# Optimization experiments

Hardware: AMD Instinct MI355X
Metric: run time of the kernel (lower is better)

## Reference

```python
import jax, jax.numpy as jnp
import numpy as np

N = 100000      # nodes
E = 1600000     # edges
D_IN = 64       # input feature dim
H = 64          # hidden dim
HNUM = 128      # number of direct virtual nodes (blocks)
NCONV = 2       # layers-1 conv layers in module_list
NMLP = 2        # layers-1 virtual-node MLPs (all applied each conv iter)
NEG_SLOPE = 0.2


def setup_inputs() -> dict:
    key = jax.random.key(0)
    ks = jax.random.split(key, 16)
    s = 0.1
    inp = {
        "x": jax.random.normal(ks[0], (N, D_IN), jnp.float32),
        "edge_index": jax.random.randint(ks[1], (2, E), 0, N, dtype=jnp.int32),
        "h_blocks": jax.random.randint(ks[2], (N,), 0, HNUM, dtype=jnp.int32),
        "h_levels": jax.random.randint(ks[3], (N,), 0, 4, dtype=jnp.int32),
        "h_num": HNUM,
        # initial GATConv(input->hidden): lin weight (no bias), att_src, att_dst, out bias
        "W0": jax.random.normal(ks[4], (D_IN, H), jnp.float32) * s,
        "a_src0": jax.random.normal(ks[5], (H,), jnp.float32) * s,
        "a_dst0": jax.random.normal(ks[6], (H,), jnp.float32) * s,
        "b0": jnp.zeros((H,), jnp.float32),
        # stacked module_list GATConv(hidden->hidden) params
        "Wl": jax.random.normal(ks[7], (NCONV, H, H), jnp.float32) * s,
        "a_srcl": jax.random.normal(ks[8], (NCONV, H), jnp.float32) * s,
        "a_dstl": jax.random.normal(ks[9], (NCONV, H), jnp.float32) * s,
        "bl": jnp.zeros((NCONV, H), jnp.float32),
        # virtual node embedding, torch init constant 0
        "vn_emb": jnp.zeros((1, H), jnp.float32),
        # virtual-node MLPs: Linear->ReLU->Linear->ReLU, weights stored (in,out)
        "mlp_W1": jax.random.normal(ks[10], (NMLP, H, H), jnp.float32) * s,
        "mlp_b1": jnp.zeros((NMLP, H), jnp.float32),
        "mlp_W2": jax.random.normal(ks[11], (NMLP, H, H), jnp.float32) * s,
        "mlp_b2": jnp.zeros((NMLP, H), jnp.float32),
    }
    return inp


def gat_conv(x, src, dst, W, a_src, a_dst, b, n_nodes):
    """PyG GATConv, heads=1, concat, add_self_loops=True, negative_slope=0.2."""
    h = x @ W                                    # [N, H]
    loop = jnp.arange(n_nodes, dtype=src.dtype)
    s = jnp.concatenate([src, loop])             # [E+N]
    d = jnp.concatenate([dst, loop])
    a_s = h @ a_src                              # [N]
    a_d = h @ a_dst
    e = jax.nn.leaky_relu(a_s[s] + a_d[d], negative_slope=NEG_SLOPE)  # [E+N]
    # segment softmax over destination nodes (self loops cover every segment)
    m = jax.ops.segment_max(e, d, num_segments=n_nodes)
    w = jnp.exp(e - m[d])
    denom = jax.ops.segment_sum(w, d, num_segments=n_nodes)
    alpha = w / (denom[d] + 1e-16)               # [E+N]
    out = jax.ops.segment_sum(h[s] * alpha[:, None], d, num_segments=n_nodes)
    return out + b


def reference(x, edge_index, h_blocks, h_levels, h_num,
              W0, a_src0, a_dst0, b0, Wl, a_srcl, a_dstl, bl,
              vn_emb, mlp_W1, mlp_b1, mlp_W2, mlp_b2):
    src, dst = edge_index[0], edge_index[1]
    n_nodes = x.shape[0]
    out = gat_conv(x, src, dst, W0, a_src0, a_dst0, b0, n_nodes)
    # embedding lookup of all-zero indices == broadcast of row 0
    vn_direct = jnp.broadcast_to(vn_emb[0], (h_num, vn_emb.shape[1]))  # [HNUM, H]
    vn_root = vn_emb                                                   # [1, H]
    for l in range(NCONV):
        out = out + vn_direct[h_blocks]
        out = gat_conv(out, src, dst, Wl[l], a_srcl[l], a_dstl[l], bl[l], n_nodes)
        vn_direct = jax.ops.segment_sum(out, h_blocks, num_segments=h_num) + vn_direct
        vn_direct = vn_direct + vn_root
        vn_root = jnp.sum(vn_direct, axis=0, keepdims=True) + vn_root
        # NB: the original applies EVERY vn-MLP inside each conv iteration
        for j in range(NMLP):
            vn_direct = jax.nn.relu(jax.nn.relu(vn_direct @ mlp_W1[j] + mlp_b1[j]) @ mlp_W2[j] + mlp_b2[j])
            vn_root = jax.nn.relu(jax.nn.relu(vn_root @ mlp_W1[j] + mlp_b1[j]) @ mlp_W2[j] + mlp_b2[j])
    return out
```

## Files before the change

kernel.cpp:

```cpp
#include <hip/hip_runtime.h>
#include <hip/hip_fp16.h>
#include <math.h>

#define HD 64
#define HNUM 128
#define NMLP 2
#define BSH 8
#define MAXNB 512
#define EPB 2048
#define NPART 256

typedef unsigned int uint_t;
typedef unsigned short ushort_t;
typedef _Float16 h8 __attribute__((ext_vector_type(8)));
typedef float vf4 __attribute__((ext_vector_type(4)));

union H8U { h8 v; uint_t u[4]; };

__device__ __forceinline__ float lrelu(float x){ return fmaxf(x, 0.2f*x); }

__device__ __forceinline__ float cvt_h(uint_t wv, uint_t sh){
    __half_raw hr; hr.x = (ushort_t)(wv >> sh);
    return __half2float((__half)hr);
}
__device__ __forceinline__ uint_t pk2(float a, float b){
    return (uint_t)__half_as_ushort(__float2half_rn(a)) |
           ((uint_t)__half_as_ushort(__float2half_rn(b)) << 16);
}

__global__ __launch_bounds__(256) void k_bcnt(const int* __restrict__ dst, int* __restrict__ gb,
                                              int E, int NB){
    __shared__ int h[MAXNB];
    int t = threadIdx.x;
    for(int i=t;i<NB;i+=256) h[i] = 0;
    __syncthreads();
    for(int e = blockIdx.x*256 + t; e < E; e += gridDim.x*256)
        atomicAdd(&h[dst[e]>>BSH], 1);
    __syncthreads();
    for(int i=t;i<NB;i+=256) if(h[i]) atomicAdd(&gb[i], h[i]);
}

__global__ __launch_bounds__(512) void k_bscan(const int* __restrict__ gb, int* __restrict__ bbase,
                                               int* __restrict__ gcur, int NB){
    __shared__ int s[512];
    int t = threadIdx.x;
    int v = (t < NB) ? gb[t] : 0;
    s[t] = v; __syncthreads();
    for(int o=1;o<512;o<<=1){
        int u = (t >= o) ? s[t-o] : 0;
        __syncthreads();
        s[t] += u;
        __syncthreads();
    }
    if(t < NB){ int ex = s[t] - v; bbase[t] = ex; gcur[t] = ex; }
}

__global__ __launch_bounds__(256) void k_bin(const int* __restrict__ src, const int* __restrict__ dst,
                                             int* __restrict__ gcur, int2* __restrict__ bdata,
                                             int E, int NB){
    __shared__ int cnt[MAXNB];
    __shared__ int base[MAXNB];
    int t = threadIdx.x;
    for(int i=t;i<NB;i+=256) cnt[i] = 0;
    __syncthreads();
    int s0 = blockIdx.x*EPB;
    int sv[8], dv[8], off[8];
    #pragma unroll
    for(int i=0;i<8;i++){
        int e = s0 + i*256 + t;
        if(e < E){
            sv[i] = src[e]; dv[i] = dst[e];
            off[i] = atomicAdd(&cnt[dv[i]>>BSH], 1);
        }
    }
    __syncthreads();
    for(int i=t;i<NB;i+=256) base[i] = cnt[i] ? atomicAdd(&gcur[i], cnt[i]) : 0;
    __syncthreads();
    #pragma unroll
    for(int i=0;i<8;i++){
        int e = s0 + i*256 + t;
        if(e < E) bdata[base[dv[i]>>BSH] + off[i]] = make_int2(sv[i], dv[i]);
    }
}

__global__ __launch_bounds__(256) void k_bfuse(const int2* __restrict__ bdata, const int* __restrict__ bbase,
                                               const int* __restrict__ gb, int* __restrict__ rp,
                                               int* __restrict__ col, int n, int NB, int E){
    __shared__ int h[256];
    __shared__ int sc[256];
    int b = blockIdx.x, t = threadIdx.x;
    int beg = bbase[b], cnt = gb[b];
    h[t] = 0; __syncthreads();
    for(int i=t;i<cnt;i+=256) atomicAdd(&h[bdata[beg+i].y & 255], 1);
    __syncthreads();
    int v = h[t];
    sc[t] = v; __syncthreads();
    for(int o=1;o<256;o<<=1){
        int u = (t >= o) ? sc[t-o] : 0;
        __syncthreads();
        sc[t] += u;
        __syncthreads();
    }
    int excl = sc[t] - v;
    int node = (b<<BSH) + t;
    if(node < n) rp[node] = beg + excl;
    if(b == NB-1 && t == 255) rp[n] = E;
    __syncthreads();
    sc[t] = excl;
    __syncthreads();
    for(int i=t;i<cnt;i+=256){
        int2 e = bdata[beg+i];
        int pos = atomicAdd(&sc[e.y & 255], 1);
        col[beg + pos] = e.x;
    }
}

__global__ __launch_bounds__(256) void k_wcvt(
    const float* __restrict__ W0, const float* __restrict__ as0, const float* __restrict__ ad0,
    const float* __restrict__ Wl, const float* __restrict__ asl, const float* __restrict__ adl,
    uint4* __restrict__ Wf3, float* __restrict__ waf3)
{
    __shared__ float wa[2][64];
    int L = blockIdx.x, t = threadIdx.x;
    const float* W  = (L==0) ? W0  : Wl  + (L-1)*HD*HD;
    const float* as = (L==0) ? as0 : asl + (L-1)*HD;
    const float* ad = (L==0) ? ad0 : adl + (L-1)*HD;
    if(t < 128){
        int sd = t>>6, k = t&63;
        const float* av = sd ? ad : as;
        float acc = 0.f;
        for(int c=0;c<HD;c++) acc = fmaf(W[k*HD+c], av[c], acc);
        wa[sd][k] = acc;
    }
    __syncthreads();
    for(int it = t; it < 512; it += 256){
        int lane = it&63, s = (it>>6)&1, tile = it>>7;
        int g = lane>>4, m = lane&15, c = tile*16 + m;
        ushort_t h[8];
        #pragma unroll
        for(int i=0;i<8;i++){
            int k = s*32 + g*4 + (i&3) + 16*(i>>2);
            h[i] = __half_as_ushort(__float2half_rn(W[k*HD + c]));
        }
        uint4 q;
        q.x = (uint_t)h[0] | ((uint_t)h[1]<<16);
        q.y = (uint_t)h[2] | ((uint_t)h[3]<<16);
        q.z = (uint_t)h[4] | ((uint_t)h[5]<<16);
        q.w = (uint_t)h[6] | ((uint_t)h[7]<<16);
        Wf3[(size_t)L*512 + (tile*2+s)*64 + lane] = q;
    }
    if(t < 128){
        int lane = t&63, sd = t>>6, g = lane>>4;
        #pragma unroll
        for(int j4=0;j4<4;j4++){
            float v[4];
            #pragma unroll
            for(int e=0;e<4;e++){
                int j = j4*4 + e;
                int k = (j>>3)*32 + g*4 + (j&3) + 16*((j>>2)&1);
                v[e] = wa[sd][k];
            }
            float* dstp = waf3 + ((size_t)L*8 + sd*4 + j4)*64*4 + lane*4;
            dstp[0]=v[0]; dstp[1]=v[1]; dstp[2]=v[2]; dstp[3]=v[3];
        }
    }
}

__global__ __launch_bounds__(256) void k_gemm(
    const float* __restrict__ IN, const float* __restrict__ addrow,
    const float* __restrict__ addtab, const int* __restrict__ hb,
    const uint4* __restrict__ Wf, const float* __restrict__ waf,
    uint_t* __restrict__ Hw, float* __restrict__ AS, float* __restrict__ AD,
    int n)
{
    __shared__ ushort_t sx[4][1024];
    int t = threadIdx.x, lane = t&63, wv = t>>6;
    int g = lane>>4, m = lane&15;
    ushort_t* sb = sx[wv];

    H8U B[8];
    #pragma unroll
    for(int f=0; f<8; f++){
        uint4 q = Wf[f*64 + lane];
        B[f].u[0]=q.x; B[f].u[1]=q.y; B[f].u[2]=q.z; B[f].u[3]=q.w;
    }
    vf4 wS[4], wD[4];
    #pragma unroll
    for(int j4=0;j4<4;j4++){
        const float* ps = waf + ((size_t)0*4 + j4)*256 + lane*4;
        const float* pd = waf + ((size_t)1*4 + j4)*256 + lane*4;
        wS[j4] = vf4{ps[0],ps[1],ps[2],ps[3]};
        wD[j4] = vf4{pd[0],pd[1],pd[2],pd[3]};
    }
    float ar0=0,ar1=0,ar2=0,ar3=0;
    if(addrow){
        const float* a = &addrow[m*4];
        ar0=a[0]; ar1=a[1]; ar2=a[2]; ar3=a[3];
    }

    int ntiles = (n + 15) >> 4;
    int wgid = (blockIdx.x*256 + t) >> 6;
    int nw = gridDim.x*4;
    for(int tile = wgid; tile < ntiles; tile += nw){
        int rb = tile*16;
        #pragma unroll
        for(int p=0;p<4;p++){
            int row = p*4 + g;
            int rowc = min(rb + row, n-1);
            float4 x4 = *(const float4*)&IN[(size_t)rowc*HD + m*4];
            if(addrow){ x4.x+=ar0; x4.y+=ar1; x4.z+=ar2; x4.w+=ar3; }
            if(addtab){
                int b = hb[rowc];
                float4 a4 = *(const float4*)&addtab[b*HD + m*4];
                x4.x+=a4.x; x4.y+=a4.y; x4.z+=a4.z; x4.w+=a4.w;
            }
            uint2 pq; pq.x = pk2(x4.x, x4.y); pq.y = pk2(x4.z, x4.w);
            int idx = (row*64 + m*4) ^ ((row&7)<<3);
            *(uint2*)&sb[idx] = pq;
        }
        int xr = (m&7)<<3;
        H8U A0, A1;
        {
            uint2 c0 = *(uint2*)&sb[(m*64 +  0 + g*4) ^ xr];
            uint2 c1 = *(uint2*)&sb[(m*64 + 16 + g*4) ^ xr];
            A0.u[0]=c0.x; A0.u[1]=c0.y; A0.u[2]=c1.x; A0.u[3]=c1.y;
            uint2 c2 = *(uint2*)&sb[(m*64 + 32 + g*4) ^ xr];
            uint2 c3 = *(uint2*)&sb[(m*64 + 48 + g*4) ^ xr];
            A1.u[0]=c2.x; A1.u[1]=c2.y; A1.u[2]=c3.x; A1.u[3]=c3.y;
        }
        float t1 = 0.f, t2 = 0.f;
        #pragma unroll
        for(int i=0;i<8;i++){
            float xv = (float)A0.v[i];
            t1 = fmaf(xv, wS[i>>2][i&3], t1);
            t2 = fmaf(xv, wD[i>>2][i&3], t2);
        }
        #pragma unroll
        for(int i=0;i<8;i++){
            float xv = (float)A1.v[i];
            t1 = fmaf(xv, wS[2+(i>>2)][i&3], t1);
            t2 = fmaf(xv, wD[2+(i>>2)][i&3], t2);
        }
        t1 += __shfl_xor(t1, 16, 64); t1 += __shfl_xor(t1, 32, 64);
        t2 += __shfl_xor(t2, 16, 64); t2 += __shfl_xor(t2, 32, 64);
        if(lane < 16 && rb + lane < n){ AS[rb+lane] = t1; AD[rb+lane] = t2; }
        vf4 z = {0.f,0.f,0.f,0.f};
        vf4 a0 = __builtin_amdgcn_mfma_f32_16x16x32_f16(A0.v, B[0].v, z, 0,0,0);
        a0     = __builtin_amdgcn_mfma_f32_16x16x32_f16(A1.v, B[1].v, a0, 0,0,0);
        vf4 a1 = __builtin_amdgcn_mfma_f32_16x16x32_f16(A0.v, B[2].v, z, 0,0,0);
        a1     = __builtin_amdgcn_mfma_f32_16x16x32_f16(A1.v, B[3].v, a1, 0,0,0);
        vf4 a2 = __builtin_amdgcn_mfma_f32_16x16x32_f16(A0.v, B[4].v, z, 0,0,0);
        a2     = __builtin_amdgcn_mfma_f32_16x16x32_f16(A1.v, B[5].v, a2, 0,0,0);
        vf4 a3 = __builtin_amdgcn_mfma_f32_16x16x32_f16(A0.v, B[6].v, z, 0,0,0);
        a3     = __builtin_amdgcn_mfma_f32_16x16x32_f16(A1.v, B[7].v, a3, 0,0,0);
        #pragma unroll
        for(int rr=0;rr<4;rr++){
            int row = rb + g*4 + rr;
            if(row < n){
                Hw[(size_t)row*32 + m]      = pk2(a0[rr], a1[rr]);
                Hw[(size_t)row*32 + 16 + m] = pk2(a2[rr], a3[rr]);
            }
        }
    }
}

__global__ __launch_bounds__(256) void k_agg(
    const uint_t* __restrict__ Hb, const float* __restrict__ AS, const float* __restrict__ AD,
    const int* __restrict__ rp, const int* __restrict__ col,
    const float* __restrict__ bias, float* __restrict__ OUT, int n)
{
    int t = threadIdx.x, lane = t & 63;
    int p = lane & 15;
    int qb = lane & 48;
    int w0 = 2*p;
    int c00 = 32*(w0>>4)+(w0&15), c01 = c00+16;
    int c10 = c00+1, c11 = c00+17;
    float b00 = bias[c00], b01 = bias[c01], b10 = bias[c10], b11 = bias[c11];
    int wv  = (blockIdx.x*256 + t) >> 6;
    int nwv = gridDim.x*4;
    for(int base = wv*4; base < n; base += nwv*4){
        int dq = min(base + (qb>>4), n-1);
        float ad = AD[dq];
        float wself = __expf(lrelu(AS[dq] + ad));
        uint2 hd = *(const uint2*)&Hb[(size_t)dq*32 + w0];
        float4 acc;
        acc.x = cvt_h(hd.x,0)*wself; acc.y = cvt_h(hd.x,16)*wself;
        acc.z = cvt_h(hd.y,0)*wself; acc.w = cvt_h(hd.y,16)*wself;
        float sacc = 0.f;
        int beg = rp[dq], end = rp[dq+1];
        int cnt = end - beg;
        int nit = (cnt + 15) >> 4;
        nit = max(nit, __shfl_xor(nit, 16, 64));
        nit = max(nit, __shfl_xor(nit, 32, 64));
        for(int it = 0; it < nit; it++){
            int j = beg + it*16 + p;
            bool valid = j < end;
            int sj = dq;
            if(cnt > 0) sj = col[valid ? j : end - 1];
            float wj = 0.f;
            if(valid) wj = __expf(lrelu(AS[sj] + ad));
            sacc += wj;
            int ccnt = cnt - it*16;
            ccnt = ccnt < 0 ? 0 : (ccnt > 16 ? 16 : ccnt);
            int emax = ccnt;
            emax = max(emax, __shfl_xor(emax, 16, 64));
            emax = max(emax, __shfl_xor(emax, 32, 64));
            int e = 0;
            for(; e + 4 <= emax; e += 4){
                float wq0 = __shfl(wj, qb+e,   64);
                float wq1 = __shfl(wj, qb+e+1, 64);
                float wq2 = __shfl(wj, qb+e+2, 64);
                float wq3 = __shfl(wj, qb+e+3, 64);
                int   sq0 = __shfl(sj, qb+e,   64);
                int   sq1 = __shfl(sj, qb+e+1, 64);
                int   sq2 = __shfl(sj, qb+e+2, 64);
                int   sq3 = __shfl(sj, qb+e+3, 64);
                uint2 v0 = *(const uint2*)&Hb[(size_t)sq0*32 + w0];
                uint2 v1 = *(const uint2*)&Hb[(size_t)sq1*32 + w0];
                uint2 v2 = *(const uint2*)&Hb[(size_t)sq2*32 + w0];
                uint2 v3 = *(const uint2*)&Hb[(size_t)sq3*32 + w0];
                acc.x = fmaf(wq0, cvt_h(v0.x,0),  acc.x);
                acc.y = fmaf(wq0, cvt_h(v0.x,16), acc.y);
                acc.z = fmaf(wq0, cvt_h(v0.y,0),  acc.z);
                acc.w = fmaf(wq0, cvt_h(v0.y,16), acc.w);
                acc.x = fmaf(wq1, cvt_h(v1.x,0),  acc.x);
                acc.y = fmaf(wq1, cvt_h(v1.x,16), acc.y);
                acc.z = fmaf(wq1, cvt_h(v1.y,0),  acc.z);
                acc.w = fmaf(wq1, cvt_h(v1.y,16), acc.w);
                acc.x = fmaf(wq2, cvt_h(v2.x,0),  acc.x);
                acc.y = fmaf(wq2, cvt_h(v2.x,16), acc.y);
                acc.z = fmaf(wq2, cvt_h(v2.y,0),  acc.z);
                acc.w = fmaf(wq2, cvt_h(v2.y,16), acc.w);
                acc.x = fmaf(wq3, cvt_h(v3.x,0),  acc.x);
                acc.y = fmaf(wq3, cvt_h(v3.x,16), acc.y);
                acc.z = fmaf(wq3, cvt_h(v3.y,0),  acc.z);
                acc.w = fmaf(wq3, cvt_h(v3.y,16), acc.w);
            }
            for(; e < emax; e++){
                float wq = __shfl(wj, qb+e, 64);
                int   sq = __shfl(sj, qb+e, 64);
                uint2 v = *(const uint2*)&Hb[(size_t)sq*32 + w0];
                acc.x = fmaf(wq, cvt_h(v.x,0),  acc.x);
                acc.y = fmaf(wq, cvt_h(v.x,16), acc.y);
                acc.z = fmaf(wq, cvt_h(v.y,0),  acc.z);
                acc.w = fmaf(wq, cvt_h(v.y,16), acc.w);
            }
        }
        sacc += __shfl_xor(sacc, 1, 64);
        sacc += __shfl_xor(sacc, 2, 64);
        sacc += __shfl_xor(sacc, 4, 64);
        sacc += __shfl_xor(sacc, 8, 64);
        float s = wself + sacc;
        float inv = 1.f/(s + 1e-16f);
        if(base + (qb>>4) < n){
            OUT[(size_t)dq*HD + c00] = fmaf(acc.x, inv, b00);
            OUT[(size_t)dq*HD + c01] = fmaf(acc.y, inv, b01);
            OUT[(size_t)dq*HD + c10] = fmaf(acc.z, inv, b10);
            OUT[(size_t)dq*HD + c11] = fmaf(acc.w, inv, b11);
        }
    }
}

__global__ __launch_bounds__(1024) void k_vnseg(const float* __restrict__ OUT, const int* __restrict__ hb,
                                                float* __restrict__ part, int n){
    __shared__ float acc[HNUM*HD];
    int t = threadIdx.x, lane = t & 63;
    for(int i=t;i<HNUM*HD;i+=1024) acc[i] = 0.f;
    __syncthreads();
    int wv  = (blockIdx.x*1024 + t) >> 6;
    int nwv = gridDim.x*16;
    for(int base = wv*8; base < n; base += nwv*8){
        float v[8]; int b[8];
        #pragma unroll
        for(int i=0;i<8;i++){
            int node = base + i;
            bool ok = node < n;
            v[i] = ok ? OUT[(size_t)node*HD + lane] : 0.f;
            b[i] = ok ? hb[node] : 0;
        }
        #pragma unroll
        for(int i=0;i<8;i++)
            unsafeAtomicAdd(&acc[b[i]*HD + lane], v[i]);
    }
    __syncthreads();
    float* pp = part + (size_t)blockIdx.x*HNUM*HD;
    for(int i=t;i<HNUM*HD;i+=1024) pp[i] = acc[i];
}

__global__ __launch_bounds__(64) void k_vn(
    const float* __restrict__ part, int nparts, const float* __restrict__ vne,
    const float* __restrict__ W1, const float* __restrict__ B1,
    const float* __restrict__ W2, const float* __restrict__ B2,
    float* __restrict__ vnD)
{
    __shared__ float sx[HD];
    int lane = threadIdx.x;
    int r = blockIdx.x;
    const float* pr = part + (size_t)r*HD + lane;
    float a0=0.f, a1=0.f, a2=0.f, a3=0.f;
    int pb = 0;
    for(; pb + 4 <= nparts; pb += 4){
        a0 += pr[(size_t)(pb  )*HNUM*HD];
        a1 += pr[(size_t)(pb+1)*HNUM*HD];
        a2 += pr[(size_t)(pb+2)*HNUM*HD];
        a3 += pr[(size_t)(pb+3)*HNUM*HD];
    }
    for(; pb < nparts; pb++) a0 += pr[(size_t)pb*HNUM*HD];
    float ve = vne[lane];
    float a = ((a0+a1)+(a2+a3)) + ve + ve;
    for(int j=0;j<NMLP;j++){
        const float* w1 = W1 + j*HD*HD; const float* b1 = B1 + j*HD;
        const float* w2 = W2 + j*HD*HD; const float* b2 = B2 + j*HD;
        __syncthreads();
        sx[lane] = a;
        __syncthreads();
        float t = b1[lane];
        #pragma unroll
        for(int in=0;in<HD;in++) t = fmaf(sx[in], w1[in*HD + lane], t);
        t = fmaxf(t, 0.f);
        __syncthreads();
        sx[lane] = t;
        __syncthreads();
        float u = b2[lane];
        #pragma unroll
        for(int in=0;in<HD;in++) u = fmaf(sx[in], w2[in*HD + lane], u);
        a = fmaxf(u, 0.f);
    }
    vnD[r*HD + lane] = a;
}

extern "C" void kernel_launch(void* const* d_in, const int* in_sizes, int n_in,
                              void* d_out, int out_size, void* d_ws, size_t ws_size,
                              hipStream_t stream)
{
    const float* x   = (const float*)d_in[0];
    const int*   ei  = (const int*)d_in[1];
    const int*   hb  = (const int*)d_in[2];
    const float* W0  = (const float*)d_in[5];
    const float* as0 = (const float*)d_in[6];
    const float* ad0 = (const float*)d_in[7];
    const float* b0  = (const float*)d_in[8];
    const float* Wl  = (const float*)d_in[9];
    const float* asl = (const float*)d_in[10];
    const float* adl = (const float*)d_in[11];
    const float* bl  = (const float*)d_in[12];
    const float* vne = (const float*)d_in[13];
    const float* mW1 = (const float*)d_in[14];
    const float* mb1 = (const float*)d_in[15];
    const float* mW2 = (const float*)d_in[16];
    const float* mb2 = (const float*)d_in[17];

    int N = in_sizes[0]/HD;
    int E = in_sizes[1]/2;
    const int* src = ei;
    const int* dst = ei + E;
    int NB = (N + (1<<BSH) - 1) >> BSH;

    char* p = (char*)d_ws;
    float* f_h   = (float*)p; p += (size_t)N*HD*4;
    float* f_as  = (float*)p; p += (size_t)N*4;
    float* f_ad  = (float*)p; p += (size_t)N*4;
    float* f_vnD = (float*)p; p += HNUM*HD*4;
    int*   i_rp  = (int*)p;   p += (size_t)(N+1)*4;
    int*   i_gb  = (int*)p;   p += MAXNB*4;
    int*   i_bb  = (int*)p;   p += MAXNB*4;
    int*   i_gc  = (int*)p;   p += MAXNB*4;
    int*   i_col = (int*)p;   p += (size_t)E*4;
    uint4* Wf3   = (uint4*)p; p += 3*512*16;
    float* waf3  = (float*)p; p += 3*8*64*4*4;
    int2*  bdata = (int2*)f_h;
    uint_t* Hw   = (uint_t*)f_h;
    float* f_part = (float*)((char*)f_h + (size_t)N*128);

    float* outb = (float*)d_out;

    k_wcvt<<<3, 256, 0, stream>>>(W0, as0, ad0, Wl, asl, adl, Wf3, waf3);

    hipMemsetAsync(i_gb, 0, MAXNB*4, stream);
    k_bcnt <<<512, 256, 0, stream>>>(dst, i_gb, E, NB);
    k_bscan<<<1, 512, 0, stream>>>(i_gb, i_bb, i_gc, NB);
    k_bin  <<<(E+EPB-1)/EPB, 256, 0, stream>>>(src, dst, i_gc, bdata, E, NB);
    k_bfuse<<<NB, 256, 0, stream>>>(bdata, i_bb, i_gb, i_rp, i_col, N, NB, E);

    int ga = 4096;
    int gg = 768;
    k_gemm<<<gg, 256, 0, stream>>>(x, nullptr, nullptr, hb, Wf3, waf3, Hw, f_as, f_ad, N);
    k_agg <<<ga, 256, 0, stream>>>(Hw, f_as, f_ad, i_rp, i_col, b0, outb, N);
    k_gemm<<<gg, 256, 0, stream>>>(outb, vne, nullptr, hb, Wf3 + 512, waf3 + 2048, Hw, f_as, f_ad, N);
    k_agg <<<ga, 256, 0, stream>>>(Hw, f_as, f_ad, i_rp, i_col, bl, outb, N);
    k_vnseg<<<NPART, 1024, 0, stream>>>(outb, hb, f_part, N);
    k_vn  <<<HNUM, 64, 0, stream>>>(f_part, NPART, vne, mW1, mb1, mW2, mb2, f_vnD);
    k_gemm<<<gg, 256, 0, stream>>>(outb, nullptr, f_vnD, hb, Wf3 + 1024, waf3 + 4096, Hw, f_as, f_ad, N);
    k_agg <<<ga, 256, 0, stream>>>(Hw, f_as, f_ad, i_rp, i_col, bl + HD, outb, N);
}
```

Measured before the change: 301.1 us.

## Replace atomic LDS segment-sum with CSR-grouped virtual-node gather reduction

Builds a per-block node permutation (count, scan, bin by h_blocks) so each virtual-node segment sum becomes a gather-reduce over its member nodes. Eight blocks per segment accumulate in registers and atomically add into a single HNUM×H buffer. This replaces 256 per-block LDS-atomic partial tables and the later 256-way partial reduction in k_vn. It adds three small preprocessing kernels and random-row gathers of the output features.

```diff
diff --git a/kernel.cpp b/kernel.cpp
--- a/kernel.cpp
+++ b/kernel.cpp
@@ -8,7 +8,6 @@
 #define BSH 8
 #define MAXNB 512
 #define EPB 2048
-#define NPART 256
 
 typedef unsigned int uint_t;
 typedef unsigned short ushort_t;
@@ -112,6 +111,57 @@
         int2 e = bdata[beg+i];
         int pos = atomicAdd(&sc[e.y & 255], 1);
         col[beg + pos] = e.x;
+    }
+}
+
+__global__ __launch_bounds__(256) void k_vcnt(const int* __restrict__ hb, int* __restrict__ vcnt, int n){
+    __shared__ int h[HNUM];
+    int t = threadIdx.x;
+    if(t < HNUM) h[t] = 0;
+    __syncthreads();
+    for(int i = blockIdx.x*256 + t; i < n; i += gridDim.x*256) atomicAdd(&h[hb[i]], 1);
+    __syncthreads();
+    if(t < HNUM && h[t]) atomicAdd(&vcnt[t], h[t]);
+}
+
+__global__ __launch_bounds__(128) void k_vscan(const int* __restrict__ vcnt, int* __restrict__ vrp,
+                                               int* __restrict__ vcur, int n){
+    __shared__ int s[HNUM];
+    int t = threadIdx.x;
+    int v = vcnt[t];
+    s[t] = v; __syncthreads();
+    for(int o=1;o<HNUM;o<<=1){
+        int u = (t >= o) ? s[t-o] : 0;
+        __syncthreads();
+        s[t] += u;
+        __syncthreads();
+    }
+    int ex = s[t] - v;
+    vrp[t] = ex; vcur[t] = ex;
+    if(t == HNUM-1) vrp[HNUM] = n;
+}
+
+__global__ __launch_bounds__(256) void k_vbin(const int* __restrict__ hb, int* __restrict__ vcur,
+                                              int* __restrict__ perm, int n){
+    __shared__ int cnt[HNUM];
+    __shared__ int base[HNUM];
+    int t = threadIdx.x;
+    if(t < HNUM) cnt[t] = 0;
+    __syncthreads();
+    int s0 = blockIdx.x*2048;
+    int hv[8], off[8];
+    #pragma unroll
+    for(int i=0;i<8;i++){
+        int nd = s0 + i*256 + t;
+        if(nd < n){ hv[i] = hb[nd]; off[i] = atomicAdd(&cnt[hv[i]], 1); }
+    }
+    __syncthreads();
+    if(t < HNUM) base[t] = cnt[t] ? atomicAdd(&vcur[t], cnt[t]) : 0;
+    __syncthreads();
+    #pragma unroll
+    for(int i=0;i<8;i++){
+        int nd = s0 + i*256 + t;
+        if(nd < n) perm[base[hv[i]] + off[i]] = nd;
     }
 }
 
@@ -361,34 +411,28 @@
     }
 }
 
-__global__ __launch_bounds__(1024) void k_vnseg(const float* __restrict__ OUT, const int* __restrict__ hb,
-                                                float* __restrict__ part, int n){
-    __shared__ float acc[HNUM*HD];
-    int t = threadIdx.x, lane = t & 63;
-    for(int i=t;i<HNUM*HD;i+=1024) acc[i] = 0.f;
-    __syncthreads();
-    int wv  = (blockIdx.x*1024 + t) >> 6;
-    int nwv = gridDim.x*16;
-    for(int base = wv*8; base < n; base += nwv*8){
-        float v[8]; int b[8];
-        #pragma unroll
-        for(int i=0;i<8;i++){
-            int node = base + i;
-            bool ok = node < n;
-            v[i] = ok ? OUT[(size_t)node*HD + lane] : 0.f;
-            b[i] = ok ? hb[node] : 0;
-        }
-        #pragma unroll
-        for(int i=0;i<8;i++)
-            unsafeAtomicAdd(&acc[b[i]*HD + lane], v[i]);
-    }
-    __syncthreads();
-    float* pp = part + (size_t)blockIdx.x*HNUM*HD;
-    for(int i=t;i<HNUM*HD;i+=1024) pp[i] = acc[i];
+__global__ __launch_bounds__(256) void k_vsum(const float* __restrict__ OUT, const int* __restrict__ perm,
+                                              const int* __restrict__ vrp, float* __restrict__ vnS){
+    int t = threadIdx.x, lane = t & 63, w = t >> 6;
+    int g = blockIdx.x >> 3, sub = blockIdx.x & 7;
+    int wig = sub*4 + w;
+    int beg = vrp[g], end = vrp[g+1];
+    float a0=0.f, a1=0.f, a2=0.f, a3=0.f;
+    int i = beg + wig;
+    for(; i + 96 < end; i += 128){
+        int p0 = perm[i], p1 = perm[i+32], p2 = perm[i+64], p3 = perm[i+96];
+        a0 += OUT[(size_t)p0*HD + lane];
+        a1 += OUT[(size_t)p1*HD + lane];
+        a2 += OUT[(size_t)p2*HD + lane];
+        a3 += OUT[(size_t)p3*HD + lane];
+    }
+    for(; i < end; i += 32) a0 += OUT[(size_t)perm[i]*HD + lane];
+    float a = (a0+a1)+(a2+a3);
+    unsafeAtomicAdd(&vnS[g*HD + lane], a);
 }
 
 __global__ __launch_bounds__(64) void k_vn(
-    const float* __restrict__ part, int nparts, const float* __restrict__ vne,
+    const float* __restrict__ vnS, const float* __restrict__ vne,
     const float* __restrict__ W1, const float* __restrict__ B1,
     const float* __restrict__ W2, const float* __restrict__ B2,
     float* __restrict__ vnD)
@@ -396,18 +440,8 @@
     __shared__ float sx[HD];
     int lane = threadIdx.x;
     int r = blockIdx.x;
-    const float* pr = part + (size_t)r*HD + lane;
-    float a0=0.f, a1=0.f, a2=0.f, a3=0.f;
-    int pb = 0;
-    for(; pb + 4 <= nparts; pb += 4){
-        a0 += pr[(size_t)(pb  )*HNUM*HD];
-        a1 += pr[(size_t)(pb+1)*HNUM*HD];
-        a2 += pr[(size_t)(pb+2)*HNUM*HD];
-        a3 += pr[(size_t)(pb+3)*HNUM*HD];
-    }
-    for(; pb < nparts; pb++) a0 += pr[(size_t)pb*HNUM*HD];
     float ve = vne[lane];
-    float a = ((a0+a1)+(a2+a3)) + ve + ve;
+    float a = vnS[r*HD + lane] + ve + ve;
     for(int j=0;j<NMLP;j++){
         const float* w1 = W1 + j*HD*HD; const float* b1 = B1 + j*HD;
         const float* w2 = W2 + j*HD*HD; const float* b2 = B2 + j*HD;
@@ -461,6 +495,11 @@
     float* f_as  = (float*)p; p += (size_t)N*4;
     float* f_ad  = (float*)p; p += (size_t)N*4;
     float* f_vnD = (float*)p; p += HNUM*HD*4;
+    float* f_vnS = (float*)p; p += HNUM*HD*4;
+    int*   i_vcnt= (int*)p;   p += HNUM*4;
+    int*   i_vrp = (int*)p;   p += (HNUM+1)*4;
+    int*   i_vcur= (int*)p;   p += HNUM*4;
+    int*   i_perm= (int*)p;   p += (size_t)N*4;
     int*   i_rp  = (int*)p;   p += (size_t)(N+1)*4;
     int*   i_gb  = (int*)p;   p += MAXNB*4;
     int*   i_bb  = (int*)p;   p += MAXNB*4;
@@ -470,17 +509,20 @@
     float* waf3  = (float*)p; p += 3*8*64*4*4;
     int2*  bdata = (int2*)f_h;
     uint_t* Hw   = (uint_t*)f_h;
-    float* f_part = (float*)((char*)f_h + (size_t)N*128);
 
     float* outb = (float*)d_out;
 
     k_wcvt<<<3, 256, 0, stream>>>(W0, as0, ad0, Wl, asl, adl, Wf3, waf3);
 
     hipMemsetAsync(i_gb, 0, MAXNB*4, stream);
+    hipMemsetAsync(f_vnS, 0, HNUM*HD*4 + HNUM*4, stream);
     k_bcnt <<<512, 256, 0, stream>>>(dst, i_gb, E, NB);
     k_bscan<<<1, 512, 0, stream>>>(i_gb, i_bb, i_gc, NB);
     k_bin  <<<(E+EPB-1)/EPB, 256, 0, stream>>>(src, dst, i_gc, bdata, E, NB);
     k_bfuse<<<NB, 256, 0, stream>>>(bdata, i_bb, i_gb, i_rp, i_col, N, NB, E);
+    k_vcnt <<<128, 256, 0, stream>>>(hb, i_vcnt, N);
+    k_vscan<<<1, 128, 0, stream>>>(i_vcnt, i_vrp, i_vcur, N);
+    k_vbin <<<(N+2047)/2048, 256, 0, stream>>>(hb, i_vcur, i_perm, N);
 
     int ga = 4096;
     int gg = 768;
@@ -488,8 +530,8 @@
     k_agg <<<ga, 256, 0, stream>>>(Hw, f_as, f_ad, i_rp, i_col, b0, outb, N);
     k_gemm<<<gg, 256, 0, stream>>>(outb, vne, nullptr, hb, Wf3 + 512, waf3 + 2048, Hw, f_as, f_ad, N);
     k_agg <<<ga, 256, 0, stream>>>(Hw, f_as, f_ad, i_rp, i_col, bl, outb, N);
-    k_vnseg<<<NPART, 1024, 0, stream>>>(outb, hb, f_part, N);
-    k_vn  <<<HNUM, 64, 0, stream>>>(f_part, NPART, vne, mW1, mb1, mW2, mb2, f_vnD);
+    k_vsum<<<HNUM*8, 256, 0, stream>>>(outb, i_perm, i_vrp, f_vnS);
+    k_vn  <<<HNUM, 64, 0, stream>>>(f_vnS, vne, mW1, mb1, mW2, mb2, f_vnD);
     k_gemm<<<gg, 256, 0, stream>>>(outb, nullptr, f_vnD, hb, Wf3 + 1024, waf3 + 4096, Hw, f_as, f_ad, N);
     k_agg <<<ga, 256, 0, stream>>>(Hw, f_as, f_ad, i_rp, i_col, bl + HD, outb, N);
 }
```

New measurement: 262.0 us. -13.0%, faster.
